# Kernel tuning notes

Measured on AMD Instinct MI355X. Metric: run time of the kernel, lower is better.

The kernel has to match this reference:

```python
import jax, jax.numpy as jnp
import numpy as np

SIGMA = 300.0      # args.sigma (temporal gaussian kernel width, frames)
DECAY = 0.9        # args.memory_decay; avg() uses weight = 1/decay per older entry
W_TIME = 1.0       # args.temporal_weight
ORIG_LOSS = 1.0    # args.originalloss_weight
EPS = 1e-7         # BCE clamp


def _get_msg(bank_values, bank_times, bank_mask, ids, times, future):
    """Vectorized MessagePassing.get_msg: per-(id,time) gather of stored
    messages, temporal-kernel + decay weighted average. Mirrors avg():
    out = sum_i dw_i * kernel_i * v_i / sum_i dw_i, dw_i = (1/decay)^rank_i
    with rank over entries passing the past/future condition, zeros if empty."""
    vals = bank_values[ids]                      # [N, M, C]
    ts = bank_times[ids].astype(jnp.float32)     # [N, M]
    mk = bank_mask[ids]                          # [N, M]
    t0 = times.astype(jnp.float32)[:, None]      # [N, 1]
    cond = (ts > t0) if future else (ts < t0)
    m = (mk & cond).astype(vals.dtype)           # [N, M]
    kern = jnp.exp(-((ts - t0) ** 2) / (2.0 * SIGMA ** 2))
    rank = jnp.cumsum(m, axis=1) - m             # exclusive rank among valid entries
    dw = ((1.0 / DECAY) ** rank) * m             # decay weights, masked
    num = jnp.einsum('nm,nmc->nc', dw * kern, vals)
    den = jnp.sum(dw, axis=1, keepdims=True)     # denominator excludes kernel (as avg())
    msg = jnp.where(den > 0, num / jnp.maximum(den, EPS), 0.0)
    return msg * W_TIME


def _bce(p, t):
    p = jnp.clip(p, EPS, 1.0 - EPS)
    return -jnp.mean(t * jnp.log(p) + (1.0 - t) * jnp.log(1.0 - p))


def setup_inputs() -> dict:
    key = jax.random.key(0)
    k = jax.random.split(key, 8)
    N, C, NUM_IDS, M = 512, 157, 10000, 20
    return {
        'a': jax.random.normal(k[0], (N, C), jnp.float32),
        'aa': jax.random.normal(k[1], (N, C, C), jnp.float32),
        'target': jax.random.uniform(k[2], (N, C), jnp.float32),
        'bank_values': jax.random.uniform(k[3], (NUM_IDS, M, C), jnp.float32),
        'bank_times': jax.random.randint(k[4], (NUM_IDS, M), 0, 1000, jnp.int32),
        'bank_mask': jnp.ones((NUM_IDS, M), dtype=bool),
        'ids': jax.random.randint(k[5], (N,), 0, NUM_IDS, jnp.int32),
        'times': jax.random.randint(k[6], (N,), 0, 1000, jnp.int32),
    }


def reference(a, aa, target, bank_values, bank_times, bank_mask, ids, times):
    # msg/fmsg come from stored (detached) data in the original
    msg = jax.lax.stop_gradient(_get_msg(bank_values, bank_times, bank_mask, ids, times, future=False))
    fmsg = jax.lax.stop_gradient(_get_msg(bank_values, bank_times, bank_mask, ids, times, future=True))
    # qa = a + sum_i aa[n,i,j]*msg[n,i] + sum_j aa[n,i,j]*fmsg[n,j]
    qa = a + jnp.einsum('nij,ni->nj', aa, msg) + jnp.einsum('nij,nj->ni', aa, fmsg)
    qa = jax.nn.sigmoid(qa)
    loss = _bce(qa, target) + _bce(jax.nn.sigmoid(a), target) * ORIG_LOSS
    # training, adjustment=False: pastloss = futureloss = 0
    loss = loss / 3.0
    return qa, loss
```

## Files before the change

kernel.cpp:

```cpp
#include <hip/hip_runtime.h>
#include <math.h>

#define N 512
#define C 157
#define M 20
#define NW 8

__device__ __forceinline__ float sigmoidf_(float x) {
    return 1.0f / (1.0f + __expf(-x));
}
__device__ __forceinline__ float ntload(const float* p) {
    return __builtin_nontemporal_load(p);
}

__global__ __launch_bounds__(512) void atf_main_kernel(
    const float* __restrict__ a,
    const float* __restrict__ aa,
    const float* __restrict__ target,
    const float* __restrict__ bank_values,
    const int* __restrict__ bank_times,
    const int* __restrict__ bank_mask,
    const int* __restrict__ ids,
    const int* __restrict__ times,
    float* __restrict__ out,
    float* __restrict__ loss_part)
{
    const int n    = blockIdx.x;
    const int tid  = threadIdx.x;
    const int wave = tid >> 6;
    const int lane = tid & 63;

    __shared__ float s_ts[M];
    __shared__ int   s_mk[M];
    __shared__ float s_msg[C];
    __shared__ float s_fmsg[C];
    __shared__ float s_row[C];
    __shared__ float s_colp[NW][C];
    __shared__ float s_red[NW];

    const int   id = ids[n];
    const float t0 = (float)times[n];

    if (tid < M) {
        s_ts[tid] = (float)bank_times[(size_t)id * M + tid];
        s_mk[tid] = (bank_mask[(size_t)id * M + tid] != 0) ? 1 : 0;
    }
    __syncthreads();

    if (tid < C) {
        const float inv2s2 = 1.0f / (2.0f * 300.0f * 300.0f);
        const float INVDEC = 1.0f / 0.9f;
        float accP = 0.f, accF = 0.f, denP = 0.f, denF = 0.f;
        float wP = 1.f, wF = 1.f;
        const float* vb = bank_values + (size_t)id * M * C + tid;
        #pragma unroll
        for (int m = 0; m < M; ++m) {
            const float ts = s_ts[m];
            const float d  = ts - t0;
            const float kern = __expf(-d * d * inv2s2);
            const float v = vb[m * C];
            const bool mk = (s_mk[m] != 0);
            if (mk && ts < t0) { accP += wP * kern * v; denP += wP; wP *= INVDEC; }
            if (mk && ts > t0) { accF += wF * kern * v; denF += wF; wF *= INVDEC; }
        }
        s_msg[tid]  = (denP > 0.f) ? accP / fmaxf(denP, 1e-7f) : 0.0f;
        s_fmsg[tid] = (denF > 0.f) ? accF / fmaxf(denF, 1e-7f) : 0.0f;
    }
    __syncthreads();

    const float* aan = aa + (size_t)n * C * C;
    const int j0 = lane, j1 = lane + 64, j2 = lane + 128;
    float col0 = 0.f, col1 = 0.f, col2 = 0.f;
    const bool ok1 = (j1 < C), ok2 = (j2 < C);
    const float f0 = s_fmsg[j0];
    const float f1 = ok1 ? s_fmsg[j1] : 0.0f;
    const float f2 = ok2 ? s_fmsg[j2] : 0.0f;

    for (int i = wave; i < C; i += 2 * NW) {
        const int ib = i + NW;
        const float* rowA = aan + i * C;
        const float mA = s_msg[i];
        const float a0 = ntload(rowA + j0);
        const float a1 = ok1 ? ntload(rowA + j1) : 0.0f;
        const float a2 = ok2 ? ntload(rowA + j2) : 0.0f;

        float b0 = 0.f, b1 = 0.f, b2 = 0.f, mB = 0.f;
        if (ib < C) {
            const float* rowB = aan + ib * C;
            mB = s_msg[ib];
            b0 = ntload(rowB + j0);
            b1 = ok1 ? ntload(rowB + j1) : 0.0f;
            b2 = ok2 ? ntload(rowB + j2) : 0.0f;
        }

        col0 += a0 * mA + b0 * mB;
        col1 += a1 * mA + b1 * mB;
        col2 += a2 * mA + b2 * mB;

        float rpA = a0 * f0 + a1 * f1 + a2 * f2;
        float rpB = b0 * f0 + b1 * f1 + b2 * f2;
        #pragma unroll
        for (int off = 32; off > 0; off >>= 1) {
            rpA += __shfl_down(rpA, off, 64);
            rpB += __shfl_down(rpB, off, 64);
        }
        if (lane == 0) {
            s_row[i] = rpA;
            if (ib < C) s_row[ib] = rpB;
        }
    }
    s_colp[wave][j0] = col0;
    if (ok1) s_colp[wave][j1] = col1;
    if (ok2) s_colp[wave][j2] = col2;
    __syncthreads();

    float local = 0.0f;
    if (tid < C) {
        float colsum = 0.0f;
        #pragma unroll
        for (int w = 0; w < NW; ++w) colsum += s_colp[w][tid];
        const float av = a[(size_t)n * C + tid];
        const float qlin = av + colsum + s_row[tid];
        const float p = sigmoidf_(qlin);
        out[(size_t)n * C + tid] = p;

        const float t = target[(size_t)n * C + tid];
        float pc = fminf(fmaxf(p, 1e-7f), 1.0f - 1e-7f);
        float pa = sigmoidf_(av);
        pa = fminf(fmaxf(pa, 1e-7f), 1.0f - 1e-7f);
        local = t * logf(pc) + (1.0f - t) * logf(1.0f - pc)
              + t * logf(pa) + (1.0f - t) * logf(1.0f - pa);
    }
    #pragma unroll
    for (int off = 32; off > 0; off >>= 1) local += __shfl_down(local, off, 64);
    if (lane == 0) s_red[wave] = local;
    __syncthreads();
    if (tid == 0) {
        float s = 0.0f;
        #pragma unroll
        for (int w = 0; w < NW; ++w) s += s_red[w];
        loss_part[n] = s;
    }
}

__global__ __launch_bounds__(256) void atf_finalize_kernel(
    const float* __restrict__ loss_part,
    float* __restrict__ out)
{
    const int tid  = threadIdx.x;
    const int wave = tid >> 6;
    const int lane = tid & 63;
    __shared__ double s_red[4];

    double local = (double)loss_part[tid] + (double)loss_part[tid + 256];
    #pragma unroll
    for (int off = 32; off > 0; off >>= 1) local += __shfl_down(local, off, 64);
    if (lane == 0) s_red[wave] = local;
    __syncthreads();
    if (tid == 0) {
        const double s = s_red[0] + s_red[1] + s_red[2] + s_red[3];
        out[N * C] = (float)(-s / ((double)(N * C) * 3.0));
    }
}

extern "C" void kernel_launch(void* const* d_in, const int* in_sizes, int n_in,
                              void* d_out, int out_size, void* d_ws, size_t ws_size,
                              hipStream_t stream) {
    const float* a           = (const float*)d_in[0];
    const float* aa          = (const float*)d_in[1];
    const float* target      = (const float*)d_in[2];
    const float* bank_values = (const float*)d_in[3];
    const int*   bank_times  = (const int*)d_in[4];
    const int*   bank_mask   = (const int*)d_in[5];
    const int*   ids         = (const int*)d_in[6];
    const int*   times       = (const int*)d_in[7];

    float* out       = (float*)d_out;
    float* loss_part = (float*)d_ws;

    atf_main_kernel<<<N, 512, 0, stream>>>(a, aa, target, bank_values, bank_times,
                                           bank_mask, ids, times, out, loss_part);
    atf_finalize_kernel<<<1, 256, 0, stream>>>(loss_part, out);
}
```

Before: 204.8 us.

## Vectorize aa row loads to float4, double waves per block, shorten row reductions

Each lane now loads four consecutive floats of an aa row through a 4-byte-aligned vector type instead of three strided scalar loads, and the block grows to 16 waves. The row dot-product reduction stops after three shuffle steps and writes 8 partial sums per row to shared memory, which are summed in the epilogue. Nontemporal loads are dropped. The intent is to issue fewer, wider memory instructions and keep more loads in flight on this bandwidth-bound 50 MB stream, at the cost of misaligned vector accesses (row stride 157 is not a multiple of 4) and more shared memory.

After: 226.6 us. 10.7% more time.

```diff
diff --git a/kernel.cpp b/kernel.cpp
--- a/kernel.cpp
+++ b/kernel.cpp
@@ -4,16 +4,16 @@
 #define N 512
 #define C 157
 #define M 20
-#define NW 8
+#define NWAVE 16
+
+typedef float float4a __attribute__((ext_vector_type(4), aligned(4)));
+typedef float float4s __attribute__((ext_vector_type(4), aligned(16)));
 
 __device__ __forceinline__ float sigmoidf_(float x) {
     return 1.0f / (1.0f + __expf(-x));
 }
-__device__ __forceinline__ float ntload(const float* p) {
-    return __builtin_nontemporal_load(p);
-}
 
-__global__ __launch_bounds__(512) void atf_main_kernel(
+__global__ __launch_bounds__(1024, 8) void atf_main_kernel(
     const float* __restrict__ a,
     const float* __restrict__ aa,
     const float* __restrict__ target,
@@ -33,10 +33,10 @@
     __shared__ float s_ts[M];
     __shared__ int   s_mk[M];
     __shared__ float s_msg[C];
-    __shared__ float s_fmsg[C];
-    __shared__ float s_row[C];
-    __shared__ float s_colp[NW][C];
-    __shared__ float s_red[NW];
+    __shared__ alignas(16) float s_fmsg[C];
+    __shared__ float s_rowp[8][C];
+    __shared__ alignas(16) float s_colp[NWAVE][160];
+    __shared__ float s_red[NWAVE];
 
     const int   id = ids[n];
     const float t0 = (float)times[n];
@@ -69,58 +69,63 @@
     __syncthreads();
 
     const float* aan = aa + (size_t)n * C * C;
-    const int j0 = lane, j1 = lane + 64, j2 = lane + 128;
-    float col0 = 0.f, col1 = 0.f, col2 = 0.f;
-    const bool ok1 = (j1 < C), ok2 = (j2 < C);
-    const float f0 = s_fmsg[j0];
-    const float f1 = ok1 ? s_fmsg[j1] : 0.0f;
-    const float f2 = ok2 ? s_fmsg[j2] : 0.0f;
+    float4s f4 = {0.f, 0.f, 0.f, 0.f};
+    if (lane < 39)       f4 = *(const float4s*)&s_fmsg[4 * lane];
+    else if (lane == 39) f4.x = s_fmsg[156];
 
-    for (int i = wave; i < C; i += 2 * NW) {
-        const int ib = i + NW;
-        const float* rowA = aan + i * C;
+    float c0 = 0.f, c1 = 0.f, c2 = 0.f, c3 = 0.f;
+
+    for (int i = wave; i < C; i += 2 * NWAVE) {
+        const int ib = i + NWAVE;
+        const float* rA = aan + i * C;
+        float4a vA = {0.f, 0.f, 0.f, 0.f};
+        if (lane < 39)       vA = *(const float4a*)(rA + 4 * lane);
+        else if (lane == 39) vA.x = rA[156];
         const float mA = s_msg[i];
-        const float a0 = ntload(rowA + j0);
-        const float a1 = ok1 ? ntload(rowA + j1) : 0.0f;
-        const float a2 = ok2 ? ntload(rowA + j2) : 0.0f;
 
-        float b0 = 0.f, b1 = 0.f, b2 = 0.f, mB = 0.f;
+        float4a vB = {0.f, 0.f, 0.f, 0.f};
+        float mB = 0.f;
         if (ib < C) {
-            const float* rowB = aan + ib * C;
+            const float* rB = aan + ib * C;
+            if (lane < 39)       vB = *(const float4a*)(rB + 4 * lane);
+            else if (lane == 39) vB.x = rB[156];
             mB = s_msg[ib];
-            b0 = ntload(rowB + j0);
-            b1 = ok1 ? ntload(rowB + j1) : 0.0f;
-            b2 = ok2 ? ntload(rowB + j2) : 0.0f;
         }
 
-        col0 += a0 * mA + b0 * mB;
-        col1 += a1 * mA + b1 * mB;
-        col2 += a2 * mA + b2 * mB;
+        c0 += vA.x * mA + vB.x * mB;
+        c1 += vA.y * mA + vB.y * mB;
+        c2 += vA.z * mA + vB.z * mB;
+        c3 += vA.w * mA + vB.w * mB;
 
-        float rpA = a0 * f0 + a1 * f1 + a2 * f2;
-        float rpB = b0 * f0 + b1 * f1 + b2 * f2;
-        #pragma unroll
-        for (int off = 32; off > 0; off >>= 1) {
-            rpA += __shfl_down(rpA, off, 64);
-            rpB += __shfl_down(rpB, off, 64);
-        }
-        if (lane == 0) {
-            s_row[i] = rpA;
-            if (ib < C) s_row[ib] = rpB;
+        float rpA = vA.x * f4.x + vA.y * f4.y + vA.z * f4.z + vA.w * f4.w;
+        float rpB = vB.x * f4.x + vB.y * f4.y + vB.z * f4.z + vB.w * f4.w;
+        rpA += __shfl_down(rpA, 32, 64);  rpB += __shfl_down(rpB, 32, 64);
+        rpA += __shfl_down(rpA, 16, 64);  rpB += __shfl_down(rpB, 16, 64);
+        rpA += __shfl_down(rpA,  8, 64);  rpB += __shfl_down(rpB,  8, 64);
+        if (lane < 8) {
+            s_rowp[lane][i] = rpA;
+            if (ib < C) s_rowp[lane][ib] = rpB;
         }
     }
-    s_colp[wave][j0] = col0;
-    if (ok1) s_colp[wave][j1] = col1;
-    if (ok2) s_colp[wave][j2] = col2;
+    if (lane < 39) {
+        float4s cv = {c0, c1, c2, c3};
+        *(float4s*)&s_colp[wave][4 * lane] = cv;
+    } else if (lane == 39) {
+        s_colp[wave][156] = c0;
+    }
     __syncthreads();
 
     float local = 0.0f;
     if (tid < C) {
         float colsum = 0.0f;
         #pragma unroll
-        for (int w = 0; w < NW; ++w) colsum += s_colp[w][tid];
+        for (int w = 0; w < NWAVE; ++w) colsum += s_colp[w][tid];
+        float rowsum = 0.0f;
+        #pragma unroll
+        for (int k = 0; k < 8; ++k) rowsum += s_rowp[k][tid];
+
         const float av = a[(size_t)n * C + tid];
-        const float qlin = av + colsum + s_row[tid];
+        const float qlin = av + colsum + rowsum;
         const float p = sigmoidf_(qlin);
         out[(size_t)n * C + tid] = p;
 
@@ -138,7 +143,7 @@
     if (tid == 0) {
         float s = 0.0f;
         #pragma unroll
-        for (int w = 0; w < NW; ++w) s += s_red[w];
+        for (int w = 0; w < NWAVE; ++w) s += s_red[w];
         loss_part[n] = s;
     }
 }
@@ -178,7 +183,7 @@
     float* out       = (float*)d_out;
     float* loss_part = (float*)d_ws;
 
-    atf_main_kernel<<<N, 512, 0, stream>>>(a, aa, target, bank_values, bank_times,
-                                           bank_mask, ids, times, out, loss_part);
+    atf_main_kernel<<<N, 1024, 0, stream>>>(a, aa, target, bank_values, bank_times,
+                                            bank_mask, ids, times, out, loss_part);
     atf_finalize_kernel<<<1, 256, 0, stream>>>(loss_part, out);
 }
```

## Prefetch aa rows before message computation and software-pipeline row loads

Applied to the files above, without the earlier changes.

Issues the first pair of aa row loads, plus a and target, before the bank gather and message computation, so HBM latency overlaps with that phase. The main loop is software-pipelined: each iteration loads the next rows while computing the current ones. The row reduction stops after three shuffle steps and writes 8 partial sums per row to shared memory, which the final stage adds up. Nontemporal loads are dropped. The cost is more live registers and extra shared memory for the partial row sums.

Result: no change. 203.5 us (-0.7%).

```diff
diff --git a/kernel.cpp b/kernel.cpp
--- a/kernel.cpp
+++ b/kernel.cpp
@@ -8,9 +8,6 @@
 
 __device__ __forceinline__ float sigmoidf_(float x) {
     return 1.0f / (1.0f + __expf(-x));
-}
-__device__ __forceinline__ float ntload(const float* p) {
-    return __builtin_nontemporal_load(p);
 }
 
 __global__ __launch_bounds__(512) void atf_main_kernel(
@@ -34,12 +31,29 @@
     __shared__ int   s_mk[M];
     __shared__ float s_msg[C];
     __shared__ float s_fmsg[C];
-    __shared__ float s_row[C];
+    __shared__ float s_rowp[8][C];
     __shared__ float s_colp[NW][C];
     __shared__ float s_red[NW];
 
     const int   id = ids[n];
     const float t0 = (float)times[n];
+
+    const float* aan = aa + (size_t)n * C * C;
+    const int j0 = lane, j1 = lane + 64, j2 = lane + 128;
+    const bool ok1 = (j1 < C), ok2 = (j2 < C);
+
+    float a0, a1, a2, b0, b1, b2;
+    {
+        const float* rA = aan + wave * C;
+        a0 = rA[j0]; a1 = ok1 ? rA[j1] : 0.0f; a2 = ok2 ? rA[j2] : 0.0f;
+        const float* rB = aan + (wave + NW) * C;
+        b0 = rB[j0]; b1 = ok1 ? rB[j1] : 0.0f; b2 = ok2 ? rB[j2] : 0.0f;
+    }
+    float av = 0.0f, tv = 0.0f;
+    if (tid < C) {
+        av = a[(size_t)n * C + tid];
+        tv = target[(size_t)n * C + tid];
+    }
 
     if (tid < M) {
         s_ts[tid] = (float)bank_times[(size_t)id * M + tid];
@@ -68,30 +82,26 @@
     }
     __syncthreads();
 
-    const float* aan = aa + (size_t)n * C * C;
-    const int j0 = lane, j1 = lane + 64, j2 = lane + 128;
     float col0 = 0.f, col1 = 0.f, col2 = 0.f;
-    const bool ok1 = (j1 < C), ok2 = (j2 < C);
     const float f0 = s_fmsg[j0];
     const float f1 = ok1 ? s_fmsg[j1] : 0.0f;
     const float f2 = ok2 ? s_fmsg[j2] : 0.0f;
 
-    for (int i = wave; i < C; i += 2 * NW) {
+    for (int i = wave; i < C; ) {
+        const int inext = i + 2 * NW;
+        float na0 = 0.f, na1 = 0.f, na2 = 0.f, nb0 = 0.f, nb1 = 0.f, nb2 = 0.f;
+        if (inext < C) {
+            const float* rA = aan + inext * C;
+            na0 = rA[j0]; na1 = ok1 ? rA[j1] : 0.0f; na2 = ok2 ? rA[j2] : 0.0f;
+            const int ibn = inext + NW;
+            if (ibn < C) {
+                const float* rB = aan + ibn * C;
+                nb0 = rB[j0]; nb1 = ok1 ? rB[j1] : 0.0f; nb2 = ok2 ? rB[j2] : 0.0f;
+            }
+        }
         const int ib = i + NW;
-        const float* rowA = aan + i * C;
         const float mA = s_msg[i];
-        const float a0 = ntload(rowA + j0);
-        const float a1 = ok1 ? ntload(rowA + j1) : 0.0f;
-        const float a2 = ok2 ? ntload(rowA + j2) : 0.0f;
-
-        float b0 = 0.f, b1 = 0.f, b2 = 0.f, mB = 0.f;
-        if (ib < C) {
-            const float* rowB = aan + ib * C;
-            mB = s_msg[ib];
-            b0 = ntload(rowB + j0);
-            b1 = ok1 ? ntload(rowB + j1) : 0.0f;
-            b2 = ok2 ? ntload(rowB + j2) : 0.0f;
-        }
+        const float mB = (ib < C) ? s_msg[ib] : 0.0f;
 
         col0 += a0 * mA + b0 * mB;
         col1 += a1 * mA + b1 * mB;
@@ -99,15 +109,16 @@
 
         float rpA = a0 * f0 + a1 * f1 + a2 * f2;
         float rpB = b0 * f0 + b1 * f1 + b2 * f2;
-        #pragma unroll
-        for (int off = 32; off > 0; off >>= 1) {
-            rpA += __shfl_down(rpA, off, 64);
-            rpB += __shfl_down(rpB, off, 64);
+        rpA += __shfl_down(rpA, 32, 64);  rpB += __shfl_down(rpB, 32, 64);
+        rpA += __shfl_down(rpA, 16, 64);  rpB += __shfl_down(rpB, 16, 64);
+        rpA += __shfl_down(rpA,  8, 64);  rpB += __shfl_down(rpB,  8, 64);
+        if (lane < 8) {
+            s_rowp[lane][i] = rpA;
+            if (ib < C) s_rowp[lane][ib] = rpB;
         }
-        if (lane == 0) {
-            s_row[i] = rpA;
-            if (ib < C) s_row[ib] = rpB;
-        }
+        a0 = na0; a1 = na1; a2 = na2;
+        b0 = nb0; b1 = nb1; b2 = nb2;
+        i = inext;
     }
     s_colp[wave][j0] = col0;
     if (ok1) s_colp[wave][j1] = col1;
@@ -119,17 +130,19 @@
         float colsum = 0.0f;
         #pragma unroll
         for (int w = 0; w < NW; ++w) colsum += s_colp[w][tid];
-        const float av = a[(size_t)n * C + tid];
-        const float qlin = av + colsum + s_row[tid];
+        float rowsum = 0.0f;
+        #pragma unroll
+        for (int k = 0; k < 8; ++k) rowsum += s_rowp[k][tid];
+
+        const float qlin = av + colsum + rowsum;
         const float p = sigmoidf_(qlin);
         out[(size_t)n * C + tid] = p;
 
-        const float t = target[(size_t)n * C + tid];
         float pc = fminf(fmaxf(p, 1e-7f), 1.0f - 1e-7f);
         float pa = sigmoidf_(av);
         pa = fminf(fmaxf(pa, 1e-7f), 1.0f - 1e-7f);
-        local = t * logf(pc) + (1.0f - t) * logf(1.0f - pc)
-              + t * logf(pa) + (1.0f - t) * logf(1.0f - pa);
+        local = tv * logf(pc) + (1.0f - tv) * logf(1.0f - pc)
+              + tv * logf(pa) + (1.0f - tv) * logf(1.0f - pa);
     }
     #pragma unroll
     for (int off = 32; off > 0; off >>= 1) local += __shfl_down(local, off, 64);
```
